# Kernel tuning notes

Hardware: AMD Instinct MI355X
Metric: run time of the kernel (lower is better)

The kernel has to match this reference:

```python
import jax, jax.numpy as jnp
import numpy as np

B, TQ, TK, D, H = 4, 2048, 2048, 512, 8  # hidden=512, num_heads=8, head_dim=64


def setup_inputs() -> dict:
    key = jax.random.key(0)
    ks = jax.random.split(key, 7)
    s = 0.03  # small init scale for linear weights
    return {
        "q": jax.random.normal(ks[0], (B, TQ, D), jnp.float32),
        "k": jax.random.normal(ks[1], (B, TK, D), jnp.float32),
        "v": jax.random.normal(ks[2], (B, TK, D), jnp.float32),
        "Wq": jax.random.normal(ks[3], (D, D), jnp.float32) * s,
        "bq": jnp.zeros((D,), jnp.float32),
        "Wk": jax.random.normal(ks[4], (D, D), jnp.float32) * s,
        "bk": jnp.zeros((D,), jnp.float32),
        "Wv": jax.random.normal(ks[5], (D, D), jnp.float32) * s,
        "bv": jnp.zeros((D,), jnp.float32),
        "Wo": jax.random.normal(ks[6], (D, D), jnp.float32) * s,
        "bo": jnp.zeros((D,), jnp.float32),
    }


def reference(q, k, v, Wq, bq, Wk, bk, Wv, bv, Wo, bo):
    Bq, Tq, _ = q.shape
    Tk = k.shape[1]
    Dh = D // H  # head dim = 64
    # torch Linear: x @ W.T + b; split heads -> [B, H, T, Dh]
    qh = (q @ Wq.T + bq).reshape(Bq, Tq, H, Dh).transpose(0, 2, 1, 3)
    kh = (k @ Wk.T + bk).reshape(Bq, Tk, H, Dh).transpose(0, 2, 1, 3)
    vh = (v @ Wv.T + bv).reshape(Bq, Tk, H, Dh).transpose(0, 2, 1, 3)
    scale = 1.0 / float(np.sqrt(Dh))
    scores = jnp.einsum("bhqd,bhkd->bhqk", qh, kh) * scale  # [B,H,Tq,Tk]
    # causal mask: tril(ones, diagonal=Tk-Tq); log-additive masking == -inf off-band
    causal = jnp.tril(jnp.ones((Tq, Tk), bool), k=Tk - Tq)
    scores = jnp.where(causal, scores, -jnp.inf)
    w = jax.nn.softmax(scores, axis=-1)  # attention weights
    x = jnp.einsum("bhqk,bhkd->bhqd", w, vh)
    x = x.transpose(0, 2, 1, 3).reshape(Bq, Tq, D)
    return x @ Wo.T + bo, w
```

## Files before the change

### kernel.cpp

```cpp
#include <hip/hip_runtime.h>


typedef __attribute__((ext_vector_type(4))) float f32x4;
typedef __attribute__((ext_vector_type(8))) short short8;
typedef __attribute__((ext_vector_type(8))) __bf16 bf16x8;
typedef __attribute__((ext_vector_type(2))) unsigned int uintx2;
typedef __attribute__((ext_vector_type(4))) unsigned int uintx4;

static __device__ __forceinline__ unsigned short bfc(float f) {
  return __builtin_bit_cast(unsigned short, (__bf16)f);
}
static __device__ __forceinline__ unsigned pkbf(float a, float b) {
  return (unsigned)bfc(a) | ((unsigned)bfc(b) << 16);
}
static __device__ __forceinline__ short8 cvt_bf8(f32x4 f0, f32x4 f1) {
  uintx4 u;
  u[0] = pkbf(f0[0], f0[1]);
  u[1] = pkbf(f0[2], f0[3]);
  u[2] = pkbf(f1[0], f1[1]);
  u[3] = pkbf(f1[2], f1[3]);
  return __builtin_bit_cast(short8, u);
}

static __device__ __forceinline__ f32x4 mfma16(short8 a, short8 b, f32x4 c) {
  return __builtin_amdgcn_mfma_f32_16x16x32_bf16(
      __builtin_bit_cast(bf16x8, a), __builtin_bit_cast(bf16x8, b), c, 0, 0, 0);
}

#define GLD16(gsrc, ldst)                                                     \
  __builtin_amdgcn_global_load_lds(                                           \
      (const __attribute__((address_space(1))) void*)(gsrc),                  \
      (__attribute__((address_space(3))) void*)(ldst), 16, 0, 0)

template <int IN_BF16>
__device__ __forceinline__ void gemm_core(const void* __restrict__ Xv,
                                          const float* __restrict__ W,
                                          short (*As)[72], short (*Bs)[72],
                                          int row0, int col0, f32x4 (&acc)[4][4]) {
  const int tid = threadIdx.x;
  const int lane = tid & 63;
  const int wv = tid >> 6, wm = wv >> 1, wn = wv & 1;
  const int g = lane >> 4, c = lane & 15;

  for (int k0 = 0; k0 < 512; k0 += 64) {
    for (int ch = tid; ch < 1024; ch += 256) {
      const int r = ch >> 3, kc = (ch & 7) * 8;
      if (IN_BF16) {
        *(short8*)&As[r][kc] =
            *(const short8*)((const short*)Xv + (size_t)(row0 + r) * 512 + k0 + kc);
      } else {
        const float* src = (const float*)Xv + (size_t)(row0 + r) * 512 + k0 + kc;
        *(short8*)&As[r][kc] = cvt_bf8(*(const f32x4*)src, *(const f32x4*)(src + 4));
      }
      {
        const float* src = W + (size_t)(col0 + r) * 512 + k0 + kc;
        *(short8*)&Bs[r][kc] = cvt_bf8(*(const f32x4*)src, *(const f32x4*)(src + 4));
      }
    }
    __syncthreads();
#pragma unroll
    for (int kk = 0; kk < 2; ++kk) {
      short8 a[4], b[4];
#pragma unroll
      for (int i = 0; i < 4; ++i) a[i] = *(const short8*)&As[wm * 64 + i * 16 + c][kk * 32 + g * 8];
#pragma unroll
      for (int i = 0; i < 4; ++i) b[i] = *(const short8*)&Bs[wn * 64 + i * 16 + c][kk * 32 + g * 8];
#pragma unroll
      for (int mi = 0; mi < 4; ++mi)
#pragma unroll
        for (int ni = 0; ni < 4; ++ni) acc[mi][ni] = mfma16(a[mi], b[ni], acc[mi][ni]);
    }
    __syncthreads();
  }
}

__global__ __launch_bounds__(256) void qkv_gemm(
    const float* __restrict__ q, const float* __restrict__ k, const float* __restrict__ v,
    const float* __restrict__ Wq, const float* __restrict__ bq,
    const float* __restrict__ Wk, const float* __restrict__ bk,
    const float* __restrict__ Wv, const float* __restrict__ bv,
    unsigned short* __restrict__ Qbf, unsigned short* __restrict__ Kbf,
    unsigned short* __restrict__ Vbf) {
  __shared__ short As[128][72];
  __shared__ short Bs[128][72];
  const int z = blockIdx.z;
  const float* X = z == 0 ? q : (z == 1 ? k : v);
  const float* W = z == 0 ? Wq : (z == 1 ? Wk : Wv);
  const float* bias = z == 0 ? bq : (z == 1 ? bk : bv);
  const int row0 = blockIdx.x * 128, col0 = blockIdx.y * 128;

  f32x4 acc[4][4] = {};
  gemm_core<0>(X, W, As, Bs, row0, col0, acc);

  const int lane = threadIdx.x & 63;
  const int wv = threadIdx.x >> 6, wm = wv >> 1, wn = wv & 1;
  const int g = lane >> 4, c = lane & 15;

  if (z < 2) {
    unsigned short* Y = z == 0 ? Qbf : Kbf;
#pragma unroll
    for (int mi = 0; mi < 4; ++mi)
#pragma unroll
      for (int ni = 0; ni < 4; ++ni) {
        const int col = col0 + wn * 64 + ni * 16 + c;
        const float bvl = bias[col];
        const int rowb = row0 + wm * 64 + mi * 16 + g * 4;
#pragma unroll
        for (int r = 0; r < 4; ++r) {
          const int row = rowb + r;
          const int bb = row >> 11, t = row & 2047;
          const int h = col >> 6, dh = col & 63;
          Y[((size_t)((bb * 8 + h) * 2048 + t) << 6) + dh] = bfc(acc[mi][ni][r] + bvl);
        }
      }
  } else {
#pragma unroll
    for (int mi = 0; mi < 4; ++mi)
#pragma unroll
      for (int ni = 0; ni < 4; ++ni) {
        const int col = col0 + wn * 64 + ni * 16 + c;
        const float bvl = bias[col];
        const int rowb = row0 + wm * 64 + mi * 16 + g * 4;
        const int bb = rowb >> 11, t = rowb & 2047;
        const int h = col >> 6, dh = col & 63;
        uintx2 pk;
        pk[0] = pkbf(acc[mi][ni][0] + bvl, acc[mi][ni][1] + bvl);
        pk[1] = pkbf(acc[mi][ni][2] + bvl, acc[mi][ni][3] + bvl);
        *(uintx2*)(Vbf + ((size_t)((bb * 8 + h) * 64 + dh) * 2048 + t)) = pk;
      }
  }
}

__global__ __launch_bounds__(256) void out_gemm(const unsigned short* __restrict__ ctx,
                                                const float* __restrict__ Wo,
                                                const float* __restrict__ bo,
                                                float* __restrict__ out) {
  __shared__ short As[128][72];
  __shared__ short Bs[128][72];
  const int row0 = blockIdx.x * 128, col0 = blockIdx.y * 128;
  f32x4 acc[4][4] = {};
  gemm_core<1>(ctx, Wo, As, Bs, row0, col0, acc);

  const int lane = threadIdx.x & 63;
  const int wv = threadIdx.x >> 6, wm = wv >> 1, wn = wv & 1;
  const int g = lane >> 4, c = lane & 15;
#pragma unroll
  for (int mi = 0; mi < 4; ++mi)
#pragma unroll
    for (int ni = 0; ni < 4; ++ni) {
      const int col = col0 + wn * 64 + ni * 16 + c;
      const float bvl = bo[col];
      const int rowb = row0 + wm * 64 + mi * 16 + g * 4;
#pragma unroll
      for (int r = 0; r < 4; ++r) out[(size_t)(rowb + r) * 512 + col] = acc[mi][ni][r] + bvl;
    }
}

__global__ __launch_bounds__(256) void attn_kernel(
    const unsigned short* __restrict__ Qb, const unsigned short* __restrict__ Kb,
    const unsigned short* __restrict__ Vtg, unsigned short* __restrict__ ctx,
    float* __restrict__ wout) {
  __shared__ short Kd[2][8192];
  __shared__ short Vd[2][8192];
  __shared__ short Ps[4][16][128];

  const int tid = threadIdx.x, lane = tid & 63, wv = tid >> 6;
  const int g = lane >> 4, c = lane & 15;
  const int sw = (c & 7) << 3;
  const int p = blockIdx.x, bh = blockIdx.y;
  const unsigned short* Qp = Qb + (size_t)bh * (2048 * 64);
  const unsigned short* Kp = Kb + (size_t)bh * (2048 * 64);
  const unsigned short* Vp = Vtg + (size_t)bh * (64 * 2048);
  const int b_ = bh >> 3, h_ = bh & 7;
  const float SCALE = 0.18033688f;

  for (int half = 0; half < 2; ++half) {
    const int t = half ? (31 - p) : p;
    const int q0 = t * 64;
    const int jmax = t >> 1;
    const int qr = q0 + wv * 16 + c;

    __syncthreads();
#pragma unroll
    for (int i = 0; i < 4; ++i) {
      const int gr = (wv * 4 + i) * 64 + lane;
      const int row = gr >> 3, slot = gr & 7;
      GLD16(Kp + ((size_t)row * 64) + ((slot ^ (row & 7)) << 3),
            (char*)Kd[0] + ((wv * 4 + i) << 10));
    }
#pragma unroll
    for (int i = 0; i < 4; ++i) {
      const int gr = (wv * 4 + i) * 64 + lane;
      const int row = gr >> 4, slot = gr & 15;
      GLD16(Vp + ((size_t)row * 2048) + ((slot ^ (row & 7)) << 3),
            (char*)Vd[0] + ((wv * 4 + i) << 10));
    }

    short8 qf[2];
    qf[0] = *(const short8*)(Qp + (size_t)qr * 64 + g * 8);
    qf[1] = *(const short8*)(Qp + (size_t)qr * 64 + 32 + g * 8);

    f32x4 O[4] = {};
    float m_r = -3.0e38f, l_r = 0.0f;

    for (int j = 0; j <= jmax; ++j) {
      __syncthreads();
      if (j < jmax) {
        const int nb = (j + 1) & 1;
#pragma unroll
        for (int i = 0; i < 4; ++i) {
          const int gr = (wv * 4 + i) * 64 + lane;
          const int row = gr >> 3, slot = gr & 7;
          GLD16(Kp + ((size_t)((j + 1) * 128 + row) * 64) + ((slot ^ (row & 7)) << 3),
                (char*)Kd[nb] + ((wv * 4 + i) << 10));
        }
#pragma unroll
        for (int i = 0; i < 4; ++i) {
          const int gr = (wv * 4 + i) * 64 + lane;
          const int row = gr >> 4, slot = gr & 15;
          GLD16(Vp + ((size_t)row * 2048) + (j + 1) * 128 + ((slot ^ (row & 7)) << 3),
                (char*)Vd[nb] + ((wv * 4 + i) << 10));
        }
      }
      const short* Ksb = Kd[j & 1];
      const short* Vsb = Vd[j & 1];

      f32x4 S[8];
#pragma unroll
      for (int nc = 0; nc < 8; ++nc) S[nc] = (f32x4){0.f, 0.f, 0.f, 0.f};
#pragma unroll
      for (int kk = 0; kk < 2; ++kk)
#pragma unroll
        for (int nc = 0; nc < 8; ++nc) {
          const int row = nc * 16 + c;
          const short8 kf = *(const short8*)&Ksb[row * 64 + (((kk * 4 + g) ^ (c & 7)) << 3)];
          S[nc] = mfma16(kf, qf[kk], S[nc]);
        }

#pragma unroll
      for (int nc = 0; nc < 8; ++nc) S[nc] *= SCALE;
      if (j == jmax) {
        const int kvb = j * 128 + g * 4;
#pragma unroll
        for (int nc = 0; nc < 8; ++nc)
#pragma unroll
          for (int r = 0; r < 4; ++r)
            if (kvb + nc * 16 + r > qr) S[nc][r] = -1.0e30f;
      }

      float mx = -1.0e30f;
#pragma unroll
      for (int nc = 0; nc < 8; ++nc)
#pragma unroll
        for (int r = 0; r < 4; ++r) mx = fmaxf(mx, S[nc][r]);
      mx = fmaxf(mx, __shfl_xor(mx, 16));
      mx = fmaxf(mx, __shfl_xor(mx, 32));
      const float mn = fmaxf(m_r, mx);
      const float sc = __builtin_amdgcn_exp2f(m_r - mn);
      m_r = mn;
      float sum = 0.f;
#pragma unroll
      for (int nc = 0; nc < 8; ++nc)
#pragma unroll
        for (int r = 0; r < 4; ++r) {
          const float pv = __builtin_amdgcn_exp2f(S[nc][r] - mn);
          S[nc][r] = pv;
          sum += pv;
        }
      sum += __shfl_xor(sum, 16);
      sum += __shfl_xor(sum, 32);
      l_r = l_r * sc + sum;

      float scr[4];
#pragma unroll
      for (int r = 0; r < 4; ++r) scr[r] = __shfl(sc, g * 4 + r);
#pragma unroll
      for (int nd = 0; nd < 4; ++nd) {
        O[nd][0] *= scr[0]; O[nd][1] *= scr[1]; O[nd][2] *= scr[2]; O[nd][3] *= scr[3];
      }

#pragma unroll
      for (int nc = 0; nc < 8; ++nc) {
        uintx2 pk;
        pk[0] = pkbf(S[nc][0], S[nc][1]);
        pk[1] = pkbf(S[nc][2], S[nc][3]);
        *(uintx2*)&Ps[wv][c][(nc * 16 + g * 4) ^ sw] = pk;
      }

#pragma unroll
      for (int kk2 = 0; kk2 < 4; ++kk2) {
        const short8 pa = *(const short8*)&Ps[wv][c][(kk2 * 32 + g * 8) ^ sw];
#pragma unroll
        for (int nd = 0; nd < 4; ++nd) {
          const int row = nd * 16 + c;
          const short8 vb = *(const short8*)&Vsb[row * 128 + (((kk2 * 4 + g) ^ (c & 7)) << 3)];
          O[nd] = mfma16(pa, vb, O[nd]);
        }
      }
    }

    {
      float lv[4];
#pragma unroll
      for (int r = 0; r < 4; ++r) lv[r] = __shfl(l_r, g * 4 + r);
#pragma unroll
      for (int r = 0; r < 4; ++r) {
        const float inv = 1.0f / lv[r];
        const int trow = q0 + wv * 16 + g * 4 + r;
        unsigned short* cp = ctx + ((size_t)(b_ * 2048 + trow) * 512) + h_ * 64;
#pragma unroll
        for (int nd = 0; nd < 4; ++nd) cp[nd * 16 + c] = bfc(O[nd][r] * inv);
      }
    }

    const float inv_l = 1.0f / l_r;
    float* wbase = wout + ((size_t)bh * 2048 + q0) * 2048;
    for (int j = jmax; j >= 0; --j) {
      __syncthreads();
      if (j > 0) {
#pragma unroll
        for (int i = 0; i < 4; ++i) {
          const int gr = (wv * 4 + i) * 64 + lane;
          const int row = gr >> 3, slot = gr & 7;
          GLD16(Kp + ((size_t)((j - 1) * 128 + row) * 64) + ((slot ^ (row & 7)) << 3),
                (char*)Kd[(j - 1) & 1] + ((wv * 4 + i) << 10));
        }
      }
      const short* Ksb = Kd[j & 1];

      f32x4 S[8];
#pragma unroll
      for (int nc = 0; nc < 8; ++nc) S[nc] = (f32x4){0.f, 0.f, 0.f, 0.f};
#pragma unroll
      for (int kk = 0; kk < 2; ++kk)
#pragma unroll
        for (int nc = 0; nc < 8; ++nc) {
          const int row = nc * 16 + c;
          const short8 kf = *(const short8*)&Ksb[row * 64 + (((kk * 4 + g) ^ (c & 7)) << 3)];
          S[nc] = mfma16(kf, qf[kk], S[nc]);
        }

      const bool lastj = (j == jmax);
      float* wr = wbase + (size_t)(wv * 16 + c) * 2048 + j * 128;
#pragma unroll
      for (int nc = 0; nc < 8; ++nc) {
        f32x4 w4;
#pragma unroll
        for (int r = 0; r < 4; ++r) {
          float val = __builtin_amdgcn_exp2f(S[nc][r] * SCALE - m_r) * inv_l;
          if (lastj && (j * 128 + nc * 16 + g * 4 + r > qr)) val = 0.f;
          w4[r] = val;
        }
        *(f32x4*)(wr + nc * 16 + g * 4) = w4;
      }
    }

    {
      const int c0 = (jmax + 1) * 128;
      const f32x4 z = {0.f, 0.f, 0.f, 0.f};
      for (int rr = wv; rr < 64; rr += 4) {
        float* rp = wbase + (size_t)rr * 2048;
        for (int x = c0 + lane * 4; x < 2048; x += 256) *(f32x4*)(rp + x) = z;
      }
    }
  }
}

extern "C" void kernel_launch(void* const* d_in, const int* in_sizes, int n_in,
                              void* d_out, int out_size, void* d_ws, size_t ws_size,
                              hipStream_t stream) {
  const float* q  = (const float*)d_in[0];
  const float* k  = (const float*)d_in[1];
  const float* v  = (const float*)d_in[2];
  const float* Wq = (const float*)d_in[3];
  const float* bq = (const float*)d_in[4];
  const float* Wk = (const float*)d_in[5];
  const float* bk = (const float*)d_in[6];
  const float* Wv = (const float*)d_in[7];
  const float* bv = (const float*)d_in[8];
  const float* Wo = (const float*)d_in[9];
  const float* bo = (const float*)d_in[10];

  unsigned short* Qbf = (unsigned short*)d_ws;
  unsigned short* Kbf = Qbf + (size_t)4194304;
  unsigned short* Vbf = Kbf + (size_t)4194304;
  unsigned short* ctx = Vbf + (size_t)4194304;

  float* out  = (float*)d_out;
  float* wout = out + (size_t)4 * 2048 * 512;

  qkv_gemm<<<dim3(64, 4, 3), 256, 0, stream>>>(q, k, v, Wq, bq, Wk, bk, Wv, bv, Qbf, Kbf, Vbf);
  attn_kernel<<<dim3(16, 32), 256, 0, stream>>>(Qbf, Kbf, Vbf, ctx, wout);
  out_gemm<<<dim3(64, 4), 256, 0, stream>>>(ctx, Wo, bo, out);
}
```

Before: 241.1 us.

## Split attention-weight recomputation into a separate kernel using per-row log-sum-exp offsets

The attention kernel no longer recomputes QK^T to write the weight matrix. It stores a per-row offset (-(max + log2 sum)), parking it in the output buffer before out_gemm overwrites it. A new w_kernel launched on a 32x32 grid reads that offset and writes the normalized weights plus zeros for the masked region. This spreads the large weight-write traffic over more blocks and folds the normalization into a single exp2. The cost is an extra launch and reloading Q/K, and the scratch use of the output buffer depends on out_gemm running later on the same stream.

```diff
diff --git a/kernel.cpp b/kernel.cpp
--- a/kernel.cpp
+++ b/kernel.cpp
@@ -156,10 +156,10 @@
     }
 }
 
-__global__ __launch_bounds__(256) void attn_kernel(
+__global__ __launch_bounds__(256) void attn1_kernel(
     const unsigned short* __restrict__ Qb, const unsigned short* __restrict__ Kb,
     const unsigned short* __restrict__ Vtg, unsigned short* __restrict__ ctx,
-    float* __restrict__ wout) {
+    float* __restrict__ offb) {
   __shared__ short Kd[2][8192];
   __shared__ short Vd[2][8192];
   __shared__ short Ps[4][16][128];
@@ -313,55 +313,87 @@
       }
     }
 
-    const float inv_l = 1.0f / l_r;
-    float* wbase = wout + ((size_t)bh * 2048 + q0) * 2048;
-    for (int j = jmax; j >= 0; --j) {
-      __syncthreads();
-      if (j > 0) {
-#pragma unroll
-        for (int i = 0; i < 4; ++i) {
-          const int gr = (wv * 4 + i) * 64 + lane;
-          const int row = gr >> 3, slot = gr & 7;
-          GLD16(Kp + ((size_t)((j - 1) * 128 + row) * 64) + ((slot ^ (row & 7)) << 3),
-                (char*)Kd[(j - 1) & 1] + ((wv * 4 + i) << 10));
-        }
-      }
-      const short* Ksb = Kd[j & 1];
-
-      f32x4 S[8];
-#pragma unroll
-      for (int nc = 0; nc < 8; ++nc) S[nc] = (f32x4){0.f, 0.f, 0.f, 0.f};
-#pragma unroll
-      for (int kk = 0; kk < 2; ++kk)
-#pragma unroll
-        for (int nc = 0; nc < 8; ++nc) {
-          const int row = nc * 16 + c;
-          const short8 kf = *(const short8*)&Ksb[row * 64 + (((kk * 4 + g) ^ (c & 7)) << 3)];
-          S[nc] = mfma16(kf, qf[kk], S[nc]);
-        }
-
-      const bool lastj = (j == jmax);
-      float* wr = wbase + (size_t)(wv * 16 + c) * 2048 + j * 128;
+    if (g == 0) offb[(size_t)bh * 2048 + qr] = -(m_r + __log2f(l_r));
+  }
+}
+
+__global__ __launch_bounds__(256) void w_kernel(
+    const unsigned short* __restrict__ Qb, const unsigned short* __restrict__ Kb,
+    const float* __restrict__ offb, float* __restrict__ wout) {
+  __shared__ short Kd[2][8192];
+
+  const int tid = threadIdx.x, lane = tid & 63, wv = tid >> 6;
+  const int g = lane >> 4, c = lane & 15;
+  const int t = blockIdx.x, bh = blockIdx.y;
+  const unsigned short* Qp = Qb + (size_t)bh * (2048 * 64);
+  const unsigned short* Kp = Kb + (size_t)bh * (2048 * 64);
+  const float SCALE = 0.18033688f;
+
+  const int q0 = t * 64;
+  const int jmax = t >> 1;
+  const int qr = q0 + wv * 16 + c;
+
+  short8 qf[2];
+  qf[0] = *(const short8*)(Qp + (size_t)qr * 64 + g * 8);
+  qf[1] = *(const short8*)(Qp + (size_t)qr * 64 + 32 + g * 8);
+  const float off = offb[(size_t)bh * 2048 + qr];
+
+#pragma unroll
+  for (int i = 0; i < 4; ++i) {
+    const int gr = (wv * 4 + i) * 64 + lane;
+    const int row = gr >> 3, slot = gr & 7;
+    GLD16(Kp + ((size_t)row * 64) + ((slot ^ (row & 7)) << 3),
+          (char*)Kd[0] + ((wv * 4 + i) << 10));
+  }
+
+  float* wbase = wout + ((size_t)bh * 2048 + q0) * 2048;
+  for (int j = 0; j <= jmax; ++j) {
+    __syncthreads();
+    if (j < jmax) {
+      const int nb = (j + 1) & 1;
+#pragma unroll
+      for (int i = 0; i < 4; ++i) {
+        const int gr = (wv * 4 + i) * 64 + lane;
+        const int row = gr >> 3, slot = gr & 7;
+        GLD16(Kp + ((size_t)((j + 1) * 128 + row) * 64) + ((slot ^ (row & 7)) << 3),
+              (char*)Kd[nb] + ((wv * 4 + i) << 10));
+      }
+    }
+    const short* Ksb = Kd[j & 1];
+
+    f32x4 S[8];
+#pragma unroll
+    for (int nc = 0; nc < 8; ++nc) S[nc] = (f32x4){0.f, 0.f, 0.f, 0.f};
+#pragma unroll
+    for (int kk = 0; kk < 2; ++kk)
 #pragma unroll
       for (int nc = 0; nc < 8; ++nc) {
-        f32x4 w4;
-#pragma unroll
-        for (int r = 0; r < 4; ++r) {
-          float val = __builtin_amdgcn_exp2f(S[nc][r] * SCALE - m_r) * inv_l;
-          if (lastj && (j * 128 + nc * 16 + g * 4 + r > qr)) val = 0.f;
-          w4[r] = val;
-        }
-        *(f32x4*)(wr + nc * 16 + g * 4) = w4;
-      }
-    }
-
-    {
-      const int c0 = (jmax + 1) * 128;
-      const f32x4 z = {0.f, 0.f, 0.f, 0.f};
-      for (int rr = wv; rr < 64; rr += 4) {
-        float* rp = wbase + (size_t)rr * 2048;
-        for (int x = c0 + lane * 4; x < 2048; x += 256) *(f32x4*)(rp + x) = z;
-      }
+        const int row = nc * 16 + c;
+        const short8 kf = *(const short8*)&Ksb[row * 64 + (((kk * 4 + g) ^ (c & 7)) << 3)];
+        S[nc] = mfma16(kf, qf[kk], S[nc]);
+      }
+
+    const bool lastj = (j == jmax);
+    float* wr = wbase + (size_t)(wv * 16 + c) * 2048 + j * 128;
+#pragma unroll
+    for (int nc = 0; nc < 8; ++nc) {
+      f32x4 w4;
+#pragma unroll
+      for (int r = 0; r < 4; ++r) {
+        float val = __builtin_amdgcn_exp2f(S[nc][r] * SCALE + off);
+        if (lastj && (j * 128 + nc * 16 + g * 4 + r > qr)) val = 0.f;
+        w4[r] = val;
+      }
+      *(f32x4*)(wr + nc * 16 + g * 4) = w4;
+    }
+  }
+
+  {
+    const int c0 = (jmax + 1) * 128;
+    const f32x4 z = {0.f, 0.f, 0.f, 0.f};
+    for (int rr = wv; rr < 64; rr += 4) {
+      float* rp = wbase + (size_t)rr * 2048;
+      for (int x = c0 + lane * 4; x < 2048; x += 256) *(f32x4*)(rp + x) = z;
     }
   }
 }
@@ -388,8 +420,10 @@
 
   float* out  = (float*)d_out;
   float* wout = out + (size_t)4 * 2048 * 512;
+  float* offb = out;
 
   qkv_gemm<<<dim3(64, 4, 3), 256, 0, stream>>>(q, k, v, Wq, bq, Wk, bk, Wv, bv, Qbf, Kbf, Vbf);
-  attn_kernel<<<dim3(16, 32), 256, 0, stream>>>(Qbf, Kbf, Vbf, ctx, wout);
+  attn1_kernel<<<dim3(16, 32), 256, 0, stream>>>(Qbf, Kbf, Vbf, ctx, offb);
+  w_kernel<<<dim3(32, 32), 256, 0, stream>>>(Qbf, Kbf, offb, wout);
   out_gemm<<<dim3(64, 4), 256, 0, stream>>>(ctx, Wo, bo, out);
 }
```

After: 264.7 us. +9.8%, slower.
